# Performance work log

Hardware: AMD Instinct MI355X
Metric: run time of the kernel (lower is better)

The kernel has to match this reference:

```python
import jax, jax.numpy as jnp
import numpy as np

V, B, P = 32, 128, 256   # views/directions, batch, max points per diagram
J = 75                   # n_elements (structure elements)
NF = 32                  # n_filters (= directions)
S2 = 25                  # stage_2_out
NU = 0.1
BN_EPS = 1e-5


def _transform(births, lifetimes):
    """UpperDiagonalThresholdedLogTransform(nu=0.1) on (birth, death) points."""
    deaths = births + lifetimes + 0.01
    inv = jnp.asarray(1.0 / np.sqrt(2.0), births.dtype)
    x = (births + deaths) * inv          # rotated 1st coord
    y = (deaths - births) * inv          # rotated 2nd coord (persistence), > 0
    y = jnp.where(y <= NU, jnp.log(y / NU) * NU + NU, y)
    return jnp.stack([x, y], axis=-1)    # [V,B,P,2]


def _batchnorm(x, gamma, beta, axis):
    mean = x.mean(axis=axis, keepdims=True)
    var = x.var(axis=axis, keepdims=True)  # biased, training-mode BN
    return (x - mean) / jnp.sqrt(var + BN_EPS) * gamma + beta


def setup_inputs() -> dict:
    key = jax.random.key(0)
    ks = jax.random.split(key, 20)
    inp = {
        "births": jax.random.uniform(ks[0], (V, B, P), jnp.float32),
        "lifetimes": jax.random.uniform(ks[1], (V, B, P), jnp.float32),
        "mask": jax.random.randint(ks[2], (V, B, P), 0, 2).astype(jnp.int32),
        # SLayerPHT params (one SLayer per view)
        "centers": jax.random.uniform(ks[3], (V, J, 2), jnp.float32),
        "sharpness": 4.0 + 0.1 * jax.random.normal(ks[4], (V, J, 2), jnp.float32),
        # stage_1: Conv1d(3->NF, k=1, no bias), Conv1d(NF->8, k=1, no bias)
        "w1": 0.1 * jax.random.normal(ks[5], (V, NF, 3), jnp.float32),
        "w2": 0.1 * jax.random.normal(ks[6], (V, 8, NF), jnp.float32),
        # stage_2: Linear(J->S2), BN(S2), Linear(S2->S2)
        "l1_w": 0.1 * jax.random.normal(ks[7], (V, S2, J), jnp.float32),
        "l1_b": 0.1 * jax.random.normal(ks[8], (V, S2), jnp.float32),
        "bn1_g": jnp.ones((V, S2), jnp.float32),
        "bn1_b": jnp.zeros((V, S2), jnp.float32),
        "l2_w": 0.1 * jax.random.normal(ks[9], (V, S2, S2), jnp.float32),
        "l2_b": 0.1 * jax.random.normal(ks[10], (V, S2), jnp.float32),
        # linear_1: Linear(V*S2 -> 500) + BN(500); linear_2: Linear(500 -> 200)
        "fc1_w": 0.05 * jax.random.normal(ks[11], (500, V * S2), jnp.float32),
        "fc1_b": 0.05 * jax.random.normal(ks[12], (500,), jnp.float32),
        "bn2_g": jnp.ones((500,), jnp.float32),
        "bn2_b": jnp.zeros((500,), jnp.float32),
        "fc2_w": 0.05 * jax.random.normal(ks[13], (200, 500), jnp.float32),
        "fc2_b": 0.05 * jax.random.normal(ks[14], (200,), jnp.float32),
    }
    return inp


def reference(births, lifetimes, mask, centers, sharpness, w1, w2,
              l1_w, l1_b, bn1_g, bn1_b, l2_w, l2_b,
              fc1_w, fc1_b, bn2_g, bn2_b, fc2_w, fc2_b):
    q = _transform(births, lifetimes)                 # [V,B,P,2]
    m = mask.astype(q.dtype)                          # [V,B,P]
    # SLayer: z[v,b,j] = sum_p m * exp(-sum_d s[v,j,d]^2 (q[v,b,p,d]-c[v,j,d])^2)
    s2 = sharpness * sharpness                        # [V,J,2]
    qa = jnp.concatenate([q * q, q, jnp.ones_like(q[..., :1])], axis=-1)  # [V,B,P,5]
    ca = jnp.concatenate([s2, -2.0 * s2 * centers,
                          (s2 * centers * centers).sum(-1, keepdims=True)], axis=-1)  # [V,J,5]
    d2 = jnp.einsum('vbpk,vjk->vbpj', qa, ca)         # squared weighted distance
    z = jnp.einsum('vbpj,vbp->vbj', jnp.exp(-d2), m)  # [V,B,J]
    # neighbor-direction stacking (n_neighbor_directions=1, cyclic): [i-1, i, i+1]
    zn = jnp.stack([jnp.roll(z, 1, axis=0), z, jnp.roll(z, -1, axis=0)], axis=2)  # [V,B,3,J]
    # stage_1: two 1x1 conv1d (no bias), then max over channels
    h = jnp.einsum('vbcj,vfc->vbfj', zn, w1)          # [V,B,NF,J]
    h = jnp.einsum('vbfj,vgf->vbgj', h, w2)           # [V,B,8,J]
    h = h.max(axis=2)                                 # [V,B,J]
    # stage_2: Linear -> BN(train) -> Linear -> ReLU (Dropout = eval identity)
    u = jnp.einsum('vbj,voj->vbo', h, l1_w) + l1_b[:, None, :]   # [V,B,S2]
    u = _batchnorm(u, bn1_g[:, None, :], bn1_b[:, None, :], axis=1)
    u = jnp.einsum('vbo,vpo->vbp', u, l2_w) + l2_b[:, None, :]
    u = jax.nn.relu(u)
    x = u.transpose(1, 0, 2).reshape(B, V * S2)       # torch.cat(x, 1)
    x = x @ fc1_w.T + fc1_b
    x = _batchnorm(x, bn2_g, bn2_b, axis=0)
    x = x @ fc2_w.T + fc2_b                           # [B,200]
    return x
```

## Files before the change

kernel.cpp:

```cpp
#include <hip/hip_runtime.h>

#define V 32
#define B 128
#define P 256
#define J 75
#define NF 32
#define S2 25

__global__ __launch_bounds__(256) void slayer_kernel(
    const float* __restrict__ births,
    const float* __restrict__ lifetimes,
    const int* __restrict__ mask,
    const float* __restrict__ centers,
    const float* __restrict__ sharpness,
    float* __restrict__ z)
{
    const int vb = blockIdx.x;
    const int v  = vb >> 7;
    const int tid = threadIdx.x;
    const int lane = tid & 63;

    __shared__ float4 pts[P];
    __shared__ int cnt;
    __shared__ float part[2][J];

    if (tid == 0) cnt = 0;
    __syncthreads();

    const float inv = 0.70710678118654752f;
    {
        const int gi = vb * P + tid;
        float b0 = births[gi];
        float l0 = lifetimes[gi];
        int   m  = mask[gi];
        float d  = b0 + l0 + 0.01f;
        float x  = (b0 + d) * inv;
        float y  = (d - b0) * inv;
        if (y <= 0.1f) y = __logf(y * 10.0f) * 0.1f + 0.1f;

        bool keep = (m != 0);
        unsigned long long bal = __ballot(keep);
        unsigned long long lt  = (1ull << lane) - 1ull;
        int prefix = __popcll(bal & lt);
        int total  = __popcll(bal);
        int base = 0;
        if (lane == 0) base = atomicAdd(&cnt, total);
        base = __shfl(base, 0, 64);
        if (keep) pts[base + prefix] = make_float4(x, y, x * x, y * y);
    }
    __syncthreads();

    const int n = cnt;
    float acc = 0.f;
    if (tid < 3 * J) {
        const int pid = tid / J;
        const int j   = tid - pid * J;
        const int cj  = (v * J + j) * 2;
        float cx = centers[cj + 0];
        float cy = centers[cj + 1];
        float sx = sharpness[cj + 0];
        float sy = sharpness[cj + 1];
        float s2x = sx * sx, s2y = sy * sy;
        float k0 = -s2x;
        float k1 = -s2y;
        float k2 = 2.0f * s2x * cx;
        float k3 = 2.0f * s2y * cy;
        float kc = -(s2x * cx * cx + s2y * cy * cy);
        const int p0 = (n * pid) / 3;
        const int p1 = (n * (pid + 1)) / 3;
        #pragma unroll 4
        for (int p = p0; p < p1; ++p) {
            float4 a = pts[p];
            float d = fmaf(k0, a.z, kc);
            d = fmaf(k1, a.w, d);
            d = fmaf(k2, a.x, d);
            d = fmaf(k3, a.y, d);
            acc += __expf(d);
        }
        if (pid > 0) part[pid - 1][j] = acc;
    }
    __syncthreads();

    if (tid < J)
        z[vb * J + tid] = acc + part[0][tid] + part[1][tid];
}

#define BCH 43
__global__ __launch_bounds__(256) void stage12_kernel(
    const float* __restrict__ z,
    const float* __restrict__ w1,
    const float* __restrict__ w2,
    const float* __restrict__ l1_w,
    const float* __restrict__ l1_b,
    float* __restrict__ u_pre)
{
    const int bb    = blockIdx.x;
    const int v     = bb / BCH;
    const int chunk = bb - v * BCH;
    const int b0    = chunk * 3;
    const int nb    = (b0 + 3 <= B) ? 3 : (B - b0);
    const int vm = (v + V - 1) & (V - 1);
    const int vp = (v + 1) & (V - 1);
    const int tid = threadIdx.x;

    __shared__ float w1s[NF * 3];
    __shared__ float w2s[8 * NF];
    __shared__ float l1ws[S2 * J];
    __shared__ float l1bs[S2];
    __shared__ float zsh[3][3 * J];
    __shared__ float hshA[3 * J];
    __shared__ float lred[3][J];

    if (tid < NF * 3) w1s[tid] = w1[v * NF * 3 + tid];
    if (tid < 8 * NF) w2s[tid] = w2[v * 8 * NF + tid];
    for (int i = tid; i < S2 * J; i += 256) l1ws[i] = l1_w[v * S2 * J + i];
    if (tid < S2) l1bs[tid] = l1_b[v * S2 + tid];

    for (int i = tid; i < nb * 3 * J; i += 256) {
        int bl    = i / (3 * J);
        int r     = i - bl * (3 * J);
        int which = r / J;
        int j     = r - which * J;
        int b     = b0 + bl;
        int vsrc  = (which == 0) ? vm : ((which == 1) ? v : vp);
        zsh[bl][which * J + j] = z[(vsrc * B + b) * J + j];
    }
    __syncthreads();

    if (tid < nb * J) {
        int bl = tid / J;
        int j  = tid - bl * J;
        float a0 = zsh[bl][0 * J + j];
        float a1 = zsh[bl][1 * J + j];
        float a2 = zsh[bl][2 * J + j];
        float hf[NF];
        #pragma unroll
        for (int f = 0; f < NF; ++f)
            hf[f] = w1s[f * 3 + 0] * a0 + w1s[f * 3 + 1] * a1 + w1s[f * 3 + 2] * a2;
        float hm = -3.4e38f;
        #pragma unroll
        for (int g = 0; g < 8; ++g) {
            float s = 0.f;
            #pragma unroll
            for (int f = 0; f < NF; ++f) s += w2s[g * NF + f] * hf[f];
            hm = fmaxf(hm, s);
        }
        hshA[bl * J + j] = hm;
    }
    __syncthreads();

    if (tid < nb * J) {
        int bl = tid / J;
        int r  = tid - bl * J;
        int o  = r / 3;
        int kk = r - o * 3;
        const float* wrow = l1ws + o * J + kk * 25;
        const float* hrow = hshA + bl * J + kk * 25;
        float acc = 0.f;
        #pragma unroll
        for (int j = 0; j < 25; ++j) acc += hrow[j] * wrow[j];
        lred[bl][r] = acc;
    }
    __syncthreads();

    if (tid < nb * S2) {
        int bl = tid / S2;
        int o  = tid - bl * S2;
        float acc = l1bs[o] + lred[bl][o * 3 + 0] + lred[bl][o * 3 + 1] + lred[bl][o * 3 + 2];
        u_pre[(v * B + b0 + bl) * S2 + o] = acc;
    }
}

__global__ __launch_bounds__(256) void bn1_l2_kernel(
    const float* __restrict__ u_pre,
    const float* __restrict__ bn1_g,
    const float* __restrict__ bn1_b,
    const float* __restrict__ l2_w,
    const float* __restrict__ l2_b,
    float* __restrict__ xT)
{
    const int v = blockIdx.x;
    const int tid = threadIdx.x;

    __shared__ float u[B * S2];
    __shared__ float w[S2 * S2];
    __shared__ float sred[8 * S2], ssred[8 * S2];
    __shared__ float sc[S2], sh[S2];

    for (int i = tid; i < B * S2; i += 256) u[i] = u_pre[v * B * S2 + i];
    for (int i = tid; i < S2 * S2; i += 256) w[i] = l2_w[v * S2 * S2 + i];
    __syncthreads();

    if (tid < 8 * S2) {
        int c = tid / S2;
        int o = tid - c * S2;
        float s = 0.f, ss = 0.f;
        #pragma unroll
        for (int b = c * 16; b < c * 16 + 16; ++b) {
            float x = u[b * S2 + o];
            s += x; ss += x * x;
        }
        sred[tid] = s; ssred[tid] = ss;
    }
    __syncthreads();

    if (tid < S2) {
        float s = 0.f, ss = 0.f;
        #pragma unroll
        for (int c = 0; c < 8; ++c) { s += sred[c * S2 + tid]; ss += ssred[c * S2 + tid]; }
        float mean = s * (1.f / B);
        float var  = ss * (1.f / B) - mean * mean;
        float istd = rsqrtf(var + 1e-5f);
        float g  = bn1_g[v * S2 + tid];
        float be = bn1_b[v * S2 + tid];
        sc[tid] = g * istd;
        sh[tid] = be - mean * g * istd;
    }
    __syncthreads();

    for (int i = tid; i < B * S2; i += 256) {
        int o = i % S2;
        u[i] = u[i] * sc[o] + sh[o];
    }
    __syncthreads();

    for (int i = tid; i < B * S2; i += 256) {
        int b = i & 127;
        int p = i >> 7;
        float acc = l2_b[v * S2 + p];
        #pragma unroll
        for (int o = 0; o < S2; ++o) acc += u[b * S2 + o] * w[p * S2 + o];
        acc = fmaxf(acc, 0.f);
        xT[(v * S2 + p) * B + b] = acc;
    }
}

__global__ __launch_bounds__(256) void fc1_bn2_kernel(
    const float* __restrict__ xT,
    const float* __restrict__ fc1_w,
    const float* __restrict__ fc1_b,
    const float* __restrict__ bn2_g,
    const float* __restrict__ bn2_b,
    float* __restrict__ y1n)
{
    const int n  = blockIdx.x;
    const int tid = threadIdx.x;
    const int kk = tid >> 7;
    const int b  = tid & 127;
    const int K  = V * S2;

    __shared__ float wsm[V * S2];
    __shared__ float pr[B];
    __shared__ float red[2][2];

    for (int i = tid; i < K; i += 256) wsm[i] = fc1_w[n * K + i];
    __syncthreads();

    float acc = 0.f;
    const float* xp = xT + kk * 400 * B + b;
    const float* wp = wsm + kk * 400;
    for (int k = 0; k < 400; ++k) acc += xp[k * B] * wp[k];

    if (kk == 1) pr[b] = acc;
    __syncthreads();

    float t = 0.f;
    if (kk == 0) {
        t = acc + pr[b] + fc1_b[n];
        const int wave = tid >> 6;
        const int lane = tid & 63;
        float s = t, ss = t * t;
        #pragma unroll
        for (int off = 32; off > 0; off >>= 1) {
            s  += __shfl_down(s,  off, 64);
            ss += __shfl_down(ss, off, 64);
        }
        if (lane == 0) { red[wave][0] = s; red[wave][1] = ss; }
    }
    __syncthreads();

    if (kk == 0) {
        float s  = red[0][0] + red[1][0];
        float ss = red[0][1] + red[1][1];
        float mean = s * (1.f / B);
        float var  = ss * (1.f / B) - mean * mean;
        float istd = rsqrtf(var + 1e-5f);
        float g   = bn2_g[n];
        float be  = bn2_b[n];
        float scl = g * istd;
        y1n[n * B + b] = t * scl + (be - mean * scl);
    }
}

__global__ __launch_bounds__(256) void fc2_kernel(
    const float* __restrict__ y1n,
    const float* __restrict__ fc2_w,
    const float* __restrict__ fc2_b,
    float* __restrict__ out)
{
    const int n2 = blockIdx.x;
    const int tid = threadIdx.x;
    const int kk = tid >> 7;
    const int b  = tid & 127;

    __shared__ float wsm[500];
    __shared__ float pr[B];
    for (int i = tid; i < 500; i += 256) wsm[i] = fc2_w[n2 * 500 + i];
    __syncthreads();

    float acc = 0.f;
    const float* yp = y1n + kk * 250 * B + b;
    const float* wp = wsm + kk * 250;
    for (int k = 0; k < 250; ++k) acc += yp[k * B] * wp[k];

    if (kk == 1) pr[b] = acc;
    __syncthreads();

    if (kk == 0)
        out[b * 200 + n2] = acc + pr[b] + fc2_b[n2];
}

extern "C" void kernel_launch(void* const* d_in, const int* in_sizes, int n_in,
                              void* d_out, int out_size, void* d_ws, size_t ws_size,
                              hipStream_t stream) {
    const float* births    = (const float*)d_in[0];
    const float* lifetimes = (const float*)d_in[1];
    const int*   mask      = (const int*)d_in[2];
    const float* centers   = (const float*)d_in[3];
    const float* sharpness = (const float*)d_in[4];
    const float* w1        = (const float*)d_in[5];
    const float* w2        = (const float*)d_in[6];
    const float* l1_w      = (const float*)d_in[7];
    const float* l1_b      = (const float*)d_in[8];
    const float* bn1_g     = (const float*)d_in[9];
    const float* bn1_b     = (const float*)d_in[10];
    const float* l2_w      = (const float*)d_in[11];
    const float* l2_b      = (const float*)d_in[12];
    const float* fc1_w     = (const float*)d_in[13];
    const float* fc1_b     = (const float*)d_in[14];
    const float* bn2_g     = (const float*)d_in[15];
    const float* bn2_b     = (const float*)d_in[16];
    const float* fc2_w     = (const float*)d_in[17];
    const float* fc2_b     = (const float*)d_in[18];
    float* out = (float*)d_out;

    float* ws    = (float*)d_ws;
    float* z     = ws;
    float* u_pre = ws + 307200;
    float* xT    = ws + 307200 + 102400;
    float* y1n   = ws + 307200 + 102400 + 102400;

    slayer_kernel <<<V * B, 256, 0, stream>>>(births, lifetimes, mask, centers, sharpness, z);
    stage12_kernel<<<V * BCH, 256, 0, stream>>>(z, w1, w2, l1_w, l1_b, u_pre);
    bn1_l2_kernel <<<V, 256, 0, stream>>>(u_pre, bn1_g, bn1_b, l2_w, l2_b, xT);
    fc1_bn2_kernel<<<500, 256, 0, stream>>>(xT, fc1_w, fc1_b, bn2_g, bn2_b, y1n);
    fc2_kernel    <<<200, 256, 0, stream>>>(y1n, fc2_w, fc2_b, out);
}
```

Before: 153.0 us.

## Fuse stage-1/2 linear with BN1 and L2 via atomic last-block reduction

```diff
diff --git a/kernel.cpp b/kernel.cpp
--- a/kernel.cpp
+++ b/kernel.cpp
@@ -13,12 +13,17 @@
     const int* __restrict__ mask,
     const float* __restrict__ centers,
     const float* __restrict__ sharpness,
-    float* __restrict__ z)
+    float* __restrict__ z,
+    int* __restrict__ zero_base)
 {
     const int vb = blockIdx.x;
     const int v  = vb >> 7;
     const int tid = threadIdx.x;
     const int lane = tid & 63;
+
+    if (vb == 0) {
+        for (int i = tid; i < 2 * V * S2 + V; i += 256) zero_base[i] = 0;
+    }
 
     __shared__ float4 pts[P];
     __shared__ int cnt;
@@ -85,20 +90,25 @@
         z[vb * J + tid] = acc + part[0][tid] + part[1][tid];
 }
 
-#define BCH 43
-__global__ __launch_bounds__(256) void stage12_kernel(
+__global__ __launch_bounds__(256) void stage2_bn_kernel(
     const float* __restrict__ z,
     const float* __restrict__ w1,
     const float* __restrict__ w2,
     const float* __restrict__ l1_w,
     const float* __restrict__ l1_b,
-    float* __restrict__ u_pre)
+    const float* __restrict__ bn1_g,
+    const float* __restrict__ bn1_b,
+    const float* __restrict__ l2_w,
+    const float* __restrict__ l2_b,
+    float* __restrict__ u_pre,
+    float* __restrict__ xT,
+    float* __restrict__ stats_sum,
+    float* __restrict__ stats_ss,
+    int* __restrict__ vcnt)
 {
-    const int bb    = blockIdx.x;
-    const int v     = bb / BCH;
-    const int chunk = bb - v * BCH;
-    const int b0    = chunk * 3;
-    const int nb    = (b0 + 3 <= B) ? 3 : (B - b0);
+    const int bb = blockIdx.x;
+    const int v  = bb >> 3;
+    const int b0 = (bb & 7) * 16;
     const int vm = (v + V - 1) & (V - 1);
     const int vp = (v + 1) & (V - 1);
     const int tid = threadIdx.x;
@@ -110,94 +120,84 @@
     __shared__ float zsh[3][3 * J];
     __shared__ float hshA[3 * J];
     __shared__ float lred[3][J];
+    __shared__ float ub16[16 * S2];
+    __shared__ float sred[8 * S2], ssred[8 * S2];
+    __shared__ int   last_flag;
+    __shared__ float ubig[B * S2];
+    __shared__ float wl2[S2 * S2];
+    __shared__ float sc[S2], sh[S2];
 
     if (tid < NF * 3) w1s[tid] = w1[v * NF * 3 + tid];
     if (tid < 8 * NF) w2s[tid] = w2[v * 8 * NF + tid];
     for (int i = tid; i < S2 * J; i += 256) l1ws[i] = l1_w[v * S2 * J + i];
     if (tid < S2) l1bs[tid] = l1_b[v * S2 + tid];
 
-    for (int i = tid; i < nb * 3 * J; i += 256) {
-        int bl    = i / (3 * J);
-        int r     = i - bl * (3 * J);
-        int which = r / J;
-        int j     = r - which * J;
-        int b     = b0 + bl;
-        int vsrc  = (which == 0) ? vm : ((which == 1) ? v : vp);
-        zsh[bl][which * J + j] = z[(vsrc * B + b) * J + j];
-    }
-    __syncthreads();
-
-    if (tid < nb * J) {
-        int bl = tid / J;
-        int j  = tid - bl * J;
-        float a0 = zsh[bl][0 * J + j];
-        float a1 = zsh[bl][1 * J + j];
-        float a2 = zsh[bl][2 * J + j];
-        float hf[NF];
-        #pragma unroll
-        for (int f = 0; f < NF; ++f)
-            hf[f] = w1s[f * 3 + 0] * a0 + w1s[f * 3 + 1] * a1 + w1s[f * 3 + 2] * a2;
-        float hm = -3.4e38f;
-        #pragma unroll
-        for (int g = 0; g < 8; ++g) {
-            float s = 0.f;
+    for (int bi = 0; bi < 16; bi += 3) {
+        const int nb = (bi + 3 <= 16) ? 3 : (16 - bi);
+        for (int i = tid; i < nb * 3 * J; i += 256) {
+            int bl    = i / (3 * J);
+            int r     = i - bl * (3 * J);
+            int which = r / J;
+            int j     = r - which * J;
+            int b     = b0 + bi + bl;
+            int vsrc  = (which == 0) ? vm : ((which == 1) ? v : vp);
+            zsh[bl][which * J + j] = z[(vsrc * B + b) * J + j];
+        }
+        __syncthreads();
+
+        if (tid < nb * J) {
+            int bl = tid / J;
+            int j  = tid - bl * J;
+            float a0 = zsh[bl][0 * J + j];
+            float a1 = zsh[bl][1 * J + j];
+            float a2 = zsh[bl][2 * J + j];
+            float hf[NF];
             #pragma unroll
-            for (int f = 0; f < NF; ++f) s += w2s[g * NF + f] * hf[f];
-            hm = fmaxf(hm, s);
-        }
-        hshA[bl * J + j] = hm;
-    }
-    __syncthreads();
-
-    if (tid < nb * J) {
-        int bl = tid / J;
-        int r  = tid - bl * J;
-        int o  = r / 3;
-        int kk = r - o * 3;
-        const float* wrow = l1ws + o * J + kk * 25;
-        const float* hrow = hshA + bl * J + kk * 25;
-        float acc = 0.f;
-        #pragma unroll
-        for (int j = 0; j < 25; ++j) acc += hrow[j] * wrow[j];
-        lred[bl][r] = acc;
-    }
-    __syncthreads();
-
-    if (tid < nb * S2) {
-        int bl = tid / S2;
-        int o  = tid - bl * S2;
-        float acc = l1bs[o] + lred[bl][o * 3 + 0] + lred[bl][o * 3 + 1] + lred[bl][o * 3 + 2];
-        u_pre[(v * B + b0 + bl) * S2 + o] = acc;
-    }
-}
-
-__global__ __launch_bounds__(256) void bn1_l2_kernel(
-    const float* __restrict__ u_pre,
-    const float* __restrict__ bn1_g,
-    const float* __restrict__ bn1_b,
-    const float* __restrict__ l2_w,
-    const float* __restrict__ l2_b,
-    float* __restrict__ xT)
-{
-    const int v = blockIdx.x;
-    const int tid = threadIdx.x;
-
-    __shared__ float u[B * S2];
-    __shared__ float w[S2 * S2];
-    __shared__ float sred[8 * S2], ssred[8 * S2];
-    __shared__ float sc[S2], sh[S2];
-
-    for (int i = tid; i < B * S2; i += 256) u[i] = u_pre[v * B * S2 + i];
-    for (int i = tid; i < S2 * S2; i += 256) w[i] = l2_w[v * S2 * S2 + i];
-    __syncthreads();
+            for (int f = 0; f < NF; ++f)
+                hf[f] = w1s[f * 3 + 0] * a0 + w1s[f * 3 + 1] * a1 + w1s[f * 3 + 2] * a2;
+            float hm = -3.4e38f;
+            #pragma unroll
+            for (int g = 0; g < 8; ++g) {
+                float s = 0.f;
+                #pragma unroll
+                for (int f = 0; f < NF; ++f) s += w2s[g * NF + f] * hf[f];
+                hm = fmaxf(hm, s);
+            }
+            hshA[bl * J + j] = hm;
+        }
+        __syncthreads();
+
+        if (tid < nb * J) {
+            int bl = tid / J;
+            int r  = tid - bl * J;
+            int o  = r / 3;
+            int kk = r - o * 3;
+            const float* wrow = l1ws + o * J + kk * 25;
+            const float* hrow = hshA + bl * J + kk * 25;
+            float a = 0.f;
+            #pragma unroll
+            for (int j = 0; j < 25; ++j) a += hrow[j] * wrow[j];
+            lred[bl][r] = a;
+        }
+        __syncthreads();
+
+        if (tid < nb * S2) {
+            int bl = tid / S2;
+            int o  = tid - bl * S2;
+            float uu = l1bs[o] + lred[bl][o * 3 + 0] + lred[bl][o * 3 + 1] + lred[bl][o * 3 + 2];
+            ub16[(bi + bl) * S2 + o] = uu;
+            u_pre[(v * B + b0 + bi + bl) * S2 + o] = uu;
+        }
+        __syncthreads();
+    }
 
     if (tid < 8 * S2) {
         int c = tid / S2;
         int o = tid - c * S2;
         float s = 0.f, ss = 0.f;
         #pragma unroll
-        for (int b = c * 16; b < c * 16 + 16; ++b) {
-            float x = u[b * S2 + o];
+        for (int b = c * 2; b < c * 2 + 2; ++b) {
+            float x = ub16[b * S2 + o];
             s += x; ss += x * x;
         }
         sred[tid] = s; ssred[tid] = ss;
@@ -208,6 +208,24 @@
         float s = 0.f, ss = 0.f;
         #pragma unroll
         for (int c = 0; c < 8; ++c) { s += sred[c * S2 + tid]; ss += ssred[c * S2 + tid]; }
+        atomicAdd(&stats_sum[v * S2 + tid], s);
+        atomicAdd(&stats_ss[v * S2 + tid], ss);
+    }
+
+    __threadfence();
+    if (tid == 0) {
+        int old = atomicAdd(&vcnt[v], 1);
+        last_flag = (old == 7);
+    }
+    __syncthreads();
+    if (!last_flag) return;
+    __threadfence();
+
+    for (int i = tid; i < B * S2; i += 256) ubig[i] = u_pre[v * B * S2 + i];
+    for (int i = tid; i < S2 * S2; i += 256) wl2[i] = l2_w[v * S2 * S2 + i];
+    if (tid < S2) {
+        float s  = stats_sum[v * S2 + tid];
+        float ss = stats_ss[v * S2 + tid];
         float mean = s * (1.f / B);
         float var  = ss * (1.f / B) - mean * mean;
         float istd = rsqrtf(var + 1e-5f);
@@ -220,7 +238,7 @@
 
     for (int i = tid; i < B * S2; i += 256) {
         int o = i % S2;
-        u[i] = u[i] * sc[o] + sh[o];
+        ubig[i] = ubig[i] * sc[o] + sh[o];
     }
     __syncthreads();
 
@@ -229,7 +247,7 @@
         int p = i >> 7;
         float acc = l2_b[v * S2 + p];
         #pragma unroll
-        for (int o = 0; o < S2; ++o) acc += u[b * S2 + o] * w[p * S2 + o];
+        for (int o = 0; o < S2; ++o) acc += ubig[b * S2 + o] * wl2[p * S2 + o];
         acc = fmaxf(acc, 0.f);
         xT[(v * S2 + p) * B + b] = acc;
     }
@@ -349,10 +367,14 @@
     float* u_pre = ws + 307200;
     float* xT    = ws + 307200 + 102400;
     float* y1n   = ws + 307200 + 102400 + 102400;
-
-    slayer_kernel <<<V * B, 256, 0, stream>>>(births, lifetimes, mask, centers, sharpness, z);
-    stage12_kernel<<<V * BCH, 256, 0, stream>>>(z, w1, w2, l1_w, l1_b, u_pre);
-    bn1_l2_kernel <<<V, 256, 0, stream>>>(u_pre, bn1_g, bn1_b, l2_w, l2_b, xT);
-    fc1_bn2_kernel<<<500, 256, 0, stream>>>(xT, fc1_w, fc1_b, bn2_g, bn2_b, y1n);
-    fc2_kernel    <<<200, 256, 0, stream>>>(y1n, fc2_w, fc2_b, out);
-}
+    float* ssum  = ws + 576000;
+    float* sss   = ws + 576800;
+    int*   vcnt  = (int*)(ws + 577600);
+
+    slayer_kernel  <<<V * B, 256, 0, stream>>>(births, lifetimes, mask, centers,
+                                               sharpness, z, (int*)ssum);
+    stage2_bn_kernel<<<256, 256, 0, stream>>>(z, w1, w2, l1_w, l1_b, bn1_g, bn1_b,
+                                              l2_w, l2_b, u_pre, xT, ssum, sss, vcnt);
+    fc1_bn2_kernel <<<500, 256, 0, stream>>>(xT, fc1_w, fc1_b, bn2_g, bn2_b, y1n);
+    fc2_kernel     <<<200, 256, 0, stream>>>(y1n, fc2_w, fc2_b, out);
+}
```

Measured after the change: 180.1 us. 1.18x slower.

## Fuse stage-1/Linear and BN/Linear2 kernels into one per-view 1024-thread kernel

Applied to the files above, without the earlier changes.

```diff
diff --git a/kernel.cpp b/kernel.cpp
--- a/kernel.cpp
+++ b/kernel.cpp
@@ -85,54 +85,45 @@
         z[vb * J + tid] = acc + part[0][tid] + part[1][tid];
 }
 
-#define BCH 43
-__global__ __launch_bounds__(256) void stage12_kernel(
+__global__ __launch_bounds__(1024) void stage2_kernel(
     const float* __restrict__ z,
     const float* __restrict__ w1,
     const float* __restrict__ w2,
     const float* __restrict__ l1_w,
     const float* __restrict__ l1_b,
-    float* __restrict__ u_pre)
+    const float* __restrict__ bn1_g,
+    const float* __restrict__ bn1_b,
+    const float* __restrict__ l2_w,
+    const float* __restrict__ l2_b,
+    float* __restrict__ xT)
 {
-    const int bb    = blockIdx.x;
-    const int v     = bb / BCH;
-    const int chunk = bb - v * BCH;
-    const int b0    = chunk * 3;
-    const int nb    = (b0 + 3 <= B) ? 3 : (B - b0);
-    const int vm = (v + V - 1) & (V - 1);
-    const int vp = (v + 1) & (V - 1);
+    const int v   = blockIdx.x;
     const int tid = threadIdx.x;
+    const int vm  = (v + V - 1) & (V - 1);
+    const int vp  = (v + 1) & (V - 1);
 
     __shared__ float w1s[NF * 3];
     __shared__ float w2s[8 * NF];
     __shared__ float l1ws[S2 * J];
     __shared__ float l1bs[S2];
-    __shared__ float zsh[3][3 * J];
-    __shared__ float hshA[3 * J];
-    __shared__ float lred[3][J];
-
-    if (tid < NF * 3) w1s[tid] = w1[v * NF * 3 + tid];
-    if (tid < 8 * NF) w2s[tid] = w2[v * 8 * NF + tid];
-    for (int i = tid; i < S2 * J; i += 256) l1ws[i] = l1_w[v * S2 * J + i];
-    if (tid < S2) l1bs[tid] = l1_b[v * S2 + tid];
-
-    for (int i = tid; i < nb * 3 * J; i += 256) {
-        int bl    = i / (3 * J);
-        int r     = i - bl * (3 * J);
-        int which = r / J;
-        int j     = r - which * J;
-        int b     = b0 + bl;
-        int vsrc  = (which == 0) ? vm : ((which == 1) ? v : vp);
-        zsh[bl][which * J + j] = z[(vsrc * B + b) * J + j];
-    }
-    __syncthreads();
-
-    if (tid < nb * J) {
-        int bl = tid / J;
-        int j  = tid - bl * J;
-        float a0 = zsh[bl][0 * J + j];
-        float a1 = zsh[bl][1 * J + j];
-        float a2 = zsh[bl][2 * J + j];
+    __shared__ float wl2[S2 * S2];
+    __shared__ float l2bs[S2];
+    __shared__ float hs[B * J];
+    __shared__ float us[B * S2];
+    __shared__ float sred[32 * S2], ssred[32 * S2];
+    __shared__ float sc[S2], sh[S2];
+
+    for (int i = tid; i < NF * 3;  i += 1024) w1s[i]  = w1[v * NF * 3 + i];
+    for (int i = tid; i < 8 * NF;  i += 1024) w2s[i]  = w2[v * 8 * NF + i];
+    for (int i = tid; i < S2 * J;  i += 1024) l1ws[i] = l1_w[v * S2 * J + i];
+    for (int i = tid; i < S2 * S2; i += 1024) wl2[i]  = l2_w[v * S2 * S2 + i];
+    if (tid < S2) { l1bs[tid] = l1_b[v * S2 + tid]; l2bs[tid] = l2_b[v * S2 + tid]; }
+    __syncthreads();
+
+    for (int t = tid; t < B * J; t += 1024) {
+        float a0 = z[vm * (B * J) + t];
+        float a1 = z[v  * (B * J) + t];
+        float a2 = z[vp * (B * J) + t];
         float hf[NF];
         #pragma unroll
         for (int f = 0; f < NF; ++f)
@@ -145,59 +136,29 @@
             for (int f = 0; f < NF; ++f) s += w2s[g * NF + f] * hf[f];
             hm = fmaxf(hm, s);
         }
-        hshA[bl * J + j] = hm;
-    }
-    __syncthreads();
-
-    if (tid < nb * J) {
-        int bl = tid / J;
-        int r  = tid - bl * J;
-        int o  = r / 3;
-        int kk = r - o * 3;
-        const float* wrow = l1ws + o * J + kk * 25;
-        const float* hrow = hshA + bl * J + kk * 25;
-        float acc = 0.f;
-        #pragma unroll
-        for (int j = 0; j < 25; ++j) acc += hrow[j] * wrow[j];
-        lred[bl][r] = acc;
-    }
-    __syncthreads();
-
-    if (tid < nb * S2) {
-        int bl = tid / S2;
-        int o  = tid - bl * S2;
-        float acc = l1bs[o] + lred[bl][o * 3 + 0] + lred[bl][o * 3 + 1] + lred[bl][o * 3 + 2];
-        u_pre[(v * B + b0 + bl) * S2 + o] = acc;
-    }
-}
-
-__global__ __launch_bounds__(256) void bn1_l2_kernel(
-    const float* __restrict__ u_pre,
-    const float* __restrict__ bn1_g,
-    const float* __restrict__ bn1_b,
-    const float* __restrict__ l2_w,
-    const float* __restrict__ l2_b,
-    float* __restrict__ xT)
-{
-    const int v = blockIdx.x;
-    const int tid = threadIdx.x;
-
-    __shared__ float u[B * S2];
-    __shared__ float w[S2 * S2];
-    __shared__ float sred[8 * S2], ssred[8 * S2];
-    __shared__ float sc[S2], sh[S2];
-
-    for (int i = tid; i < B * S2; i += 256) u[i] = u_pre[v * B * S2 + i];
-    for (int i = tid; i < S2 * S2; i += 256) w[i] = l2_w[v * S2 * S2 + i];
-    __syncthreads();
-
-    if (tid < 8 * S2) {
+        hs[t] = hm;
+    }
+    __syncthreads();
+
+    for (int t = tid; t < S2 * B; t += 1024) {
+        int o = t >> 7;
+        int b = t & 127;
+        float acc = l1bs[o];
+        const float* hrow = hs + b * J;
+        const float* wrow = l1ws + o * J;
+        #pragma unroll 5
+        for (int j = 0; j < J; ++j) acc += hrow[j] * wrow[j];
+        us[b * S2 + o] = acc;
+    }
+    __syncthreads();
+
+    if (tid < 32 * S2) {
         int c = tid / S2;
         int o = tid - c * S2;
         float s = 0.f, ss = 0.f;
         #pragma unroll
-        for (int b = c * 16; b < c * 16 + 16; ++b) {
-            float x = u[b * S2 + o];
+        for (int b = c * 4; b < c * 4 + 4; ++b) {
+            float x = us[b * S2 + o];
             s += x; ss += x * x;
         }
         sred[tid] = s; ssred[tid] = ss;
@@ -207,7 +168,7 @@
     if (tid < S2) {
         float s = 0.f, ss = 0.f;
         #pragma unroll
-        for (int c = 0; c < 8; ++c) { s += sred[c * S2 + tid]; ss += ssred[c * S2 + tid]; }
+        for (int c = 0; c < 32; ++c) { s += sred[c * S2 + tid]; ss += ssred[c * S2 + tid]; }
         float mean = s * (1.f / B);
         float var  = ss * (1.f / B) - mean * mean;
         float istd = rsqrtf(var + 1e-5f);
@@ -218,18 +179,20 @@
     }
     __syncthreads();
 
-    for (int i = tid; i < B * S2; i += 256) {
+    for (int i = tid; i < B * S2; i += 1024) {
         int o = i % S2;
-        u[i] = u[i] * sc[o] + sh[o];
-    }
-    __syncthreads();
-
-    for (int i = tid; i < B * S2; i += 256) {
-        int b = i & 127;
-        int p = i >> 7;
-        float acc = l2_b[v * S2 + p];
-        #pragma unroll
-        for (int o = 0; o < S2; ++o) acc += u[b * S2 + o] * w[p * S2 + o];
+        us[i] = us[i] * sc[o] + sh[o];
+    }
+    __syncthreads();
+
+    for (int t = tid; t < S2 * B; t += 1024) {
+        int p = t >> 7;
+        int b = t & 127;
+        float acc = l2bs[p];
+        const float* urow = us + b * S2;
+        const float* wrow = wl2 + p * S2;
+        #pragma unroll
+        for (int o = 0; o < S2; ++o) acc += urow[o] * wrow[o];
         acc = fmaxf(acc, 0.f);
         xT[(v * S2 + p) * B + b] = acc;
     }
@@ -346,13 +309,12 @@
 
     float* ws    = (float*)d_ws;
     float* z     = ws;
-    float* u_pre = ws + 307200;
-    float* xT    = ws + 307200 + 102400;
-    float* y1n   = ws + 307200 + 102400 + 102400;
+    float* xT    = ws + 307200;
+    float* y1n   = ws + 307200 + 102400;
 
     slayer_kernel <<<V * B, 256, 0, stream>>>(births, lifetimes, mask, centers, sharpness, z);
-    stage12_kernel<<<V * BCH, 256, 0, stream>>>(z, w1, w2, l1_w, l1_b, u_pre);
-    bn1_l2_kernel <<<V, 256, 0, stream>>>(u_pre, bn1_g, bn1_b, l2_w, l2_b, xT);
+    stage2_kernel <<<V, 1024, 0, stream>>>(z, w1, w2, l1_w, l1_b, bn1_g, bn1_b,
+                                           l2_w, l2_b, xT);
     fc1_bn2_kernel<<<500, 256, 0, stream>>>(xT, fc1_w, fc1_b, bn2_g, bn2_b, y1n);
     fc2_kernel    <<<200, 256, 0, stream>>>(y1n, fc2_w, fc2_b, out);
 }
```

Result: slower. 460.0 us (+200.7%).
